# Kernel optimization log

Measured on AMD Instinct MI355X. Metric: run time of the kernel, lower is better.

Reference implementation:

```python
import jax, jax.numpy as jnp
import numpy as np

N, B, E = 50000, 1, 800000
D_IN = 128      # input_size == out_size (residual)
HID = 128       # hidden_size
H = 4           # heads
C = HID // H    # per-head dim = 32
EPS = 1e-5


def setup_inputs() -> dict:
    key = jax.random.key(0)
    ks = jax.random.split(key, 16)
    s_in = 1.0 / np.sqrt(D_IN)
    s_hid = 1.0 / np.sqrt(HID)
    return {
        "x": jax.random.normal(ks[0], (N, B, D_IN), jnp.float32),
        "edge_index": jax.random.randint(ks[1], (2, E), 0, N, jnp.int64 if jax.config.jax_enable_x64 else jnp.int32),
        "edge_attr": jax.random.normal(ks[2], (E, HID), jnp.float32),
        # TransformerConv projections (weights stored torch-style [out, in])
        "Wq": jax.random.uniform(ks[3], (HID, D_IN), jnp.float32, -s_in, s_in),
        "bq": jnp.zeros((HID,), jnp.float32),
        "Wk": jax.random.uniform(ks[4], (HID, D_IN), jnp.float32, -s_in, s_in),
        "bk": jnp.zeros((HID,), jnp.float32),
        "Wv": jax.random.uniform(ks[5], (HID, D_IN), jnp.float32, -s_in, s_in),
        "bv": jnp.zeros((HID,), jnp.float32),
        "We": jax.random.uniform(ks[6], (HID, HID), jnp.float32, -s_hid, s_hid),  # lin_edge, no bias
        "Wskip": jax.random.uniform(ks[7], (HID, D_IN), jnp.float32, -s_in, s_in),
        "bskip": jnp.zeros((HID,), jnp.float32),
        "Wp": jax.random.uniform(ks[8], (HID, HID), jnp.float32, -s_hid, s_hid),   # physics_linear
        "bp": jnp.zeros((HID,), jnp.float32),
        "Wm": jax.random.uniform(ks[9], (D_IN, HID), jnp.float32, -s_hid, s_hid),  # merge_linear
        "bm": jnp.zeros((D_IN,), jnp.float32),
    }


def reference(x, edge_index, edge_attr, Wq, bq, Wk, bk, Wv, bv, We,
              Wskip, bskip, Wp, bp, Wm, bm):
    n = x.shape[0]
    src, dst = edge_index[0], edge_index[1]  # message flows src -> dst (j -> i)

    # node-wise QKV projections -> [N, B, H, C]
    q = (x @ Wq.T + bq).reshape(n, B, H, C)
    k = (x @ Wk.T + bk).reshape(n, B, H, C)
    v = (x @ Wv.T + bv).reshape(n, B, H, C)

    # edge feature projection -> [E, H, C]
    e = (edge_attr @ We.T).reshape(-1, H, C)

    # per-edge attention scores [E, B, H]
    k_j = k[src] + e[:, None]                       # [E, B, H, C]
    alpha = (q[dst] * k_j).sum(-1) / jnp.sqrt(jnp.asarray(C, x.dtype))

    # scatter-softmax over incoming edges of each dst node
    m = jax.ops.segment_max(alpha, dst, num_segments=n)      # [N, B, H]
    a = jnp.exp(alpha - m[dst])
    s = jax.ops.segment_sum(a, dst, num_segments=n)
    alpha = a / s[dst]

    # weighted scatter-add aggregation
    msg = (v[src] + e[:, None]) * alpha[..., None]           # [E, B, H, C]
    out = jax.ops.segment_sum(msg, dst, num_segments=n)      # [N, B, H, C]
    out = out.reshape(n, B, H * C)

    # root skip connection
    out = out + (x @ Wskip.T + bskip)

    # GraphResidualBlock tail
    out = jax.nn.relu(out)
    out = out @ Wp.T + bp
    # custom LayerNorm: normalize over the node dim (dim 0), weight/bias unused
    mu = out.mean(0, keepdims=True)
    sd = out.std(0, keepdims=True)
    out = (out - mu) / (sd + EPS)
    out = jax.nn.relu(out)
    out = out @ Wm.T + bm
    return out + x
```

## Files before the change

### kernel.cpp

```cpp
#include <hip/hip_runtime.h>
#include <stdint.h>

#define RS32 0.17677669529663687f
#define LDW 40

typedef short bf16x8 __attribute__((ext_vector_type(8)));
typedef float f32x4 __attribute__((ext_vector_type(4)));

__device__ __forceinline__ ushort f2bf(float f) {
  uint32_t b = __float_as_uint(f);
  b = (b + 0x7fffu + ((b >> 16) & 1u)) >> 16;
  return (ushort)b;
}
__device__ __forceinline__ float bflo(uint32_t w) { return __uint_as_float(w << 16); }
__device__ __forceinline__ float bfhi(uint32_t w) { return __uint_as_float(w & 0xffff0000u); }

__device__ __forceinline__ void stage16(ushort* hiA, ushort* loA, int r, int koff,
                                        const float* v) {
  uint32_t hu[8], lu[8];
#pragma unroll
  for (int i = 0; i < 8; ++i) {
    uint32_t b0 = __float_as_uint(v[2 * i]), b1 = __float_as_uint(v[2 * i + 1]);
    uint32_t h0m = b0 & 0xffff0000u, h1m = b1 & 0xffff0000u;
    hu[i] = (b0 >> 16) | h1m;
    float l0 = v[2 * i] - __uint_as_float(h0m);
    float l1 = v[2 * i + 1] - __uint_as_float(h1m);
    lu[i] = (__float_as_uint(l0) >> 16) | (__float_as_uint(l1) & 0xffff0000u);
  }
  *(uint4*)&hiA[r * LDW + koff]     = make_uint4(hu[0], hu[1], hu[2], hu[3]);
  *(uint4*)&hiA[r * LDW + koff + 8] = make_uint4(hu[4], hu[5], hu[6], hu[7]);
  *(uint4*)&loA[r * LDW + koff]     = make_uint4(lu[0], lu[1], lu[2], lu[3]);
  *(uint4*)&loA[r * LDW + koff + 8] = make_uint4(lu[4], lu[5], lu[6], lu[7]);
}

__launch_bounds__(256)
__global__ void gemm128_mfma_kernel(int mode,
                                    const float* __restrict__ A, const float* __restrict__ A2,
                                    const float* __restrict__ W, const float* __restrict__ bias,
                                    const float* __restrict__ mu, const float* __restrict__ inv,
                                    const float* __restrict__ X, float* __restrict__ out,
                                    float* __restrict__ sums, float* __restrict__ sumsq, int N)
{
  __shared__ ushort Ahi[128 * LDW], Alo[128 * LDW], Whi[128 * LDW], Wlo[128 * LDW];
  const int tid = threadIdx.x;
  const int nb = blockIdx.x * 128;
  const int lane = tid & 63, wv = tid >> 6;
  const int wr = (wv >> 1) * 64, wc = (wv & 1) * 64;
  const int fr = lane & 15, fq = lane >> 4;
  const int sr = tid >> 1, sk = (tid & 1) * 16;

  f32x4 acc[4][4];
#pragma unroll
  for (int m = 0; m < 4; ++m)
#pragma unroll
    for (int n = 0; n < 4; ++n) acc[m][n] = (f32x4)0.0f;

  for (int kc = 0; kc < 128; kc += 32) {
    float va[16], vw[16];
    {
      int gr = nb + sr;
      if (gr < N) {
#pragma unroll
        for (int i = 0; i < 4; ++i) {
          float4 v = *(const float4*)(A + (size_t)gr * 128 + kc + sk + i * 4);
          if (mode == 1) {
            float4 b = *(const float4*)(A2 + (size_t)gr * 128 + kc + sk + i * 4);
            v.x = fmaxf(v.x + b.x, 0.f); v.y = fmaxf(v.y + b.y, 0.f);
            v.z = fmaxf(v.z + b.z, 0.f); v.w = fmaxf(v.w + b.w, 0.f);
          } else if (mode == 2) {
            float4 m4 = *(const float4*)(mu + kc + sk + i * 4);
            float4 i4 = *(const float4*)(inv + kc + sk + i * 4);
            v.x = fmaxf((v.x - m4.x) * i4.x, 0.f); v.y = fmaxf((v.y - m4.y) * i4.y, 0.f);
            v.z = fmaxf((v.z - m4.z) * i4.z, 0.f); v.w = fmaxf((v.w - m4.w) * i4.w, 0.f);
          }
          va[i * 4 + 0] = v.x; va[i * 4 + 1] = v.y; va[i * 4 + 2] = v.z; va[i * 4 + 3] = v.w;
        }
      } else {
#pragma unroll
        for (int i = 0; i < 16; ++i) va[i] = 0.f;
      }
#pragma unroll
      for (int i = 0; i < 4; ++i) {
        float4 v = *(const float4*)(W + (size_t)sr * 128 + kc + sk + i * 4);
        vw[i * 4 + 0] = v.x; vw[i * 4 + 1] = v.y; vw[i * 4 + 2] = v.z; vw[i * 4 + 3] = v.w;
      }
    }
    if (kc) __syncthreads();
    stage16(Ahi, Alo, sr, sk, va);
    stage16(Whi, Wlo, sr, sk, vw);
    __syncthreads();

    bf16x8 ah[4], al[4], bh[4], bl[4];
#pragma unroll
    for (int m = 0; m < 4; ++m) {
      const int row = wr + m * 16 + fr;
      ah[m] = *(const bf16x8*)&Ahi[row * LDW + fq * 8];
      al[m] = *(const bf16x8*)&Alo[row * LDW + fq * 8];
    }
#pragma unroll
    for (int n = 0; n < 4; ++n) {
      const int col = wc + n * 16 + fr;
      bh[n] = *(const bf16x8*)&Whi[col * LDW + fq * 8];
      bl[n] = *(const bf16x8*)&Wlo[col * LDW + fq * 8];
    }
#pragma unroll
    for (int m = 0; m < 4; ++m)
#pragma unroll
      for (int n = 0; n < 4; ++n) {
        acc[m][n] = __builtin_amdgcn_mfma_f32_16x16x32_bf16(ah[m], bh[n], acc[m][n], 0, 0, 0);
        acc[m][n] = __builtin_amdgcn_mfma_f32_16x16x32_bf16(al[m], bh[n], acc[m][n], 0, 0, 0);
        acc[m][n] = __builtin_amdgcn_mfma_f32_16x16x32_bf16(ah[m], bl[n], acc[m][n], 0, 0, 0);
      }
  }

  float bcol[4];
#pragma unroll
  for (int n = 0; n < 4; ++n) bcol[n] = bias[wc + n * 16 + fr];
  float csum[4] = {0.f, 0.f, 0.f, 0.f}, csum2[4] = {0.f, 0.f, 0.f, 0.f};
#pragma unroll
  for (int m = 0; m < 4; ++m) {
    const int r0 = nb + wr + m * 16 + fq * 4;
#pragma unroll
    for (int r = 0; r < 4; ++r) {
      const int gr = r0 + r;
      if (gr < N) {
#pragma unroll
        for (int n = 0; n < 4; ++n) {
          const int c = wc + n * 16 + fr;
          float o = acc[m][n][r] + bcol[n];
          if (mode == 2) o += X[(size_t)gr * 128 + c];
          out[(size_t)gr * 128 + c] = o;
          if (mode == 1) { csum[n] += o; csum2[n] = fmaf(o, o, csum2[n]); }
        }
      }
    }
  }
  if (mode == 1) {
#pragma unroll
    for (int n = 0; n < 4; ++n) {
      csum[n] += __shfl_xor(csum[n], 16, 64);
      csum[n] += __shfl_xor(csum[n], 32, 64);
      csum2[n] += __shfl_xor(csum2[n], 16, 64);
      csum2[n] += __shfl_xor(csum2[n], 32, 64);
    }
    if (fq == 0) {
#pragma unroll
      for (int n = 0; n < 4; ++n) {
        atomicAdd(&sums[wc + n * 16 + fr], csum[n]);
        atomicAdd(&sumsq[wc + n * 16 + fr], csum2[n]);
      }
    }
  }
}

__launch_bounds__(256)
__global__ void gemmqkvsu_mfma_kernel(const float* __restrict__ x,
                                      const float* __restrict__ Wq, const float* __restrict__ bq,
                                      const float* __restrict__ Wk, const float* __restrict__ bk,
                                      const float* __restrict__ Wv, const float* __restrict__ bv,
                                      const float* __restrict__ Ws, const float* __restrict__ bs,
                                      const float* __restrict__ Mt, const float* __restrict__ bu,
                                      float* __restrict__ os, ushort* __restrict__ kvi,
                                      ushort* __restrict__ u, ushort* __restrict__ qb, int N)
{
  const int y = blockIdx.y;
  const float* W; const float* bias;
  if (y == 0)      { W = Wk; bias = bk; }
  else if (y == 1) { W = Wv; bias = bv; }
  else if (y == 2) { W = Ws; bias = bs; }
  else if (y == 7) { W = Wq; bias = bq; }
  else             { W = Mt + (size_t)(y - 3) * 128 * 128; bias = bu + (y - 3) * 128; }

  __shared__ ushort Ahi[128 * LDW], Alo[128 * LDW], Whi[128 * LDW], Wlo[128 * LDW];
  const int tid = threadIdx.x;
  const int nb = blockIdx.x * 128;
  const int lane = tid & 63, wv = tid >> 6;
  const int wr = (wv >> 1) * 64, wc = (wv & 1) * 64;
  const int fr = lane & 15, fq = lane >> 4;
  const int sr = tid >> 1, sk = (tid & 1) * 16;

  f32x4 acc[4][4];
#pragma unroll
  for (int m = 0; m < 4; ++m)
#pragma unroll
    for (int n = 0; n < 4; ++n) acc[m][n] = (f32x4)0.0f;

  for (int kc = 0; kc < 128; kc += 32) {
    float va[16], vw[16];
    {
      int gr = nb + sr;
      if (gr < N) {
#pragma unroll
        for (int i = 0; i < 4; ++i) {
          float4 v = *(const float4*)(x + (size_t)gr * 128 + kc + sk + i * 4);
          va[i * 4 + 0] = v.x; va[i * 4 + 1] = v.y; va[i * 4 + 2] = v.z; va[i * 4 + 3] = v.w;
        }
      } else {
#pragma unroll
        for (int i = 0; i < 16; ++i) va[i] = 0.f;
      }
#pragma unroll
      for (int i = 0; i < 4; ++i) {
        float4 v = *(const float4*)(W + (size_t)sr * 128 + kc + sk + i * 4);
        vw[i * 4 + 0] = v.x; vw[i * 4 + 1] = v.y; vw[i * 4 + 2] = v.z; vw[i * 4 + 3] = v.w;
      }
    }
    if (kc) __syncthreads();
    stage16(Ahi, Alo, sr, sk, va);
    stage16(Whi, Wlo, sr, sk, vw);
    __syncthreads();

    bf16x8 ah[4], al[4], bh[4], bl[4];
#pragma unroll
    for (int m = 0; m < 4; ++m) {
      const int row = wr + m * 16 + fr;
      ah[m] = *(const bf16x8*)&Ahi[row * LDW + fq * 8];
      al[m] = *(const bf16x8*)&Alo[row * LDW + fq * 8];
    }
#pragma unroll
    for (int n = 0; n < 4; ++n) {
      const int col = wc + n * 16 + fr;
      bh[n] = *(const bf16x8*)&Whi[col * LDW + fq * 8];
      bl[n] = *(const bf16x8*)&Wlo[col * LDW + fq * 8];
    }
#pragma unroll
    for (int m = 0; m < 4; ++m)
#pragma unroll
      for (int n = 0; n < 4; ++n) {
        acc[m][n] = __builtin_amdgcn_mfma_f32_16x16x32_bf16(ah[m], bh[n], acc[m][n], 0, 0, 0);
        acc[m][n] = __builtin_amdgcn_mfma_f32_16x16x32_bf16(al[m], bh[n], acc[m][n], 0, 0, 0);
        acc[m][n] = __builtin_amdgcn_mfma_f32_16x16x32_bf16(ah[m], bl[n], acc[m][n], 0, 0, 0);
      }
  }

  float bcol[4];
#pragma unroll
  for (int n = 0; n < 4; ++n) bcol[n] = bias[wc + n * 16 + fr];
#pragma unroll
  for (int m = 0; m < 4; ++m) {
    const int r0 = nb + wr + m * 16 + fq * 4;
#pragma unroll
    for (int r = 0; r < 4; ++r) {
      const int gr = r0 + r;
      if (gr < N) {
#pragma unroll
        for (int n = 0; n < 4; ++n) {
          const int c = wc + n * 16 + fr;
          float o = acc[m][n][r] + bcol[n];
          if (y == 2)      os[(size_t)gr * 128 + c] = o;
          else if (y == 7) qb[(size_t)gr * 128 + c] = f2bf(o);
          else if (y == 0) kvi[(size_t)gr * 256 + (c >> 2) * 8 + (c & 3)] = f2bf(o);
          else if (y == 1) kvi[(size_t)gr * 256 + (c >> 2) * 8 + 4 + (c & 3)] = f2bf(o);
          else             u[(size_t)gr * 512 + (y - 3) * 128 + c] = f2bf(o);
        }
      }
    }
  }
}

__global__ void prep_mt_kernel(const float* __restrict__ Wq, const float* __restrict__ We,
                               float* __restrict__ Mt)
{
  const int tid = threadIdx.x;
  const int jp = blockIdx.x * 2 + (tid >> 7);
  const int d = tid & 127;
  const int h = jp >> 7, j = jp & 127;
  const float* wq = Wq + (size_t)(32 * h) * 128 + d;
  const float* we = We + (size_t)(32 * h) * 128 + j;
  float acc = 0.f;
#pragma unroll 8
  for (int a = 0; a < 32; ++a) acc = fmaf(wq[a * 128], we[a * 128], acc);
  Mt[(size_t)jp * 128 + d] = acc;
}

__global__ void prep_bu_kernel(const float* __restrict__ bq, const float* __restrict__ We,
                               float* __restrict__ bu)
{
  const int jp = threadIdx.x;
  const int h = jp >> 7, j = jp & 127;
  float acc = 0.f;
  for (int a = 0; a < 32; ++a)
    acc = fmaf(bq[32 * h + a], We[(size_t)(32 * h + a) * 128 + j], acc);
  bu[jp] = acc;
}

__global__ void prep_web_kernel(const float* __restrict__ We, ushort* __restrict__ WeB)
{
  int idx = blockIdx.x * 256 + threadIdx.x;
  if (idx >= 128 * 512) return;
  int c = idx >> 9, j = idx & 511;
  int hh = j >> 7, k2 = j & 127;
  WeB[idx] = (hh == (c >> 5)) ? f2bf(We[(size_t)c * 128 + k2]) : (ushort)0;
}

__global__ void deg_kernel(const int* __restrict__ ei, int* __restrict__ deg, int E)
{
  int e = blockIdx.x * 256 + threadIdx.x;
  if (e < E) atomicAdd(&deg[ei[E + e]], 1);
}

__launch_bounds__(256)
__global__ void start_kernel(const int* __restrict__ deg, int* __restrict__ offs,
                             int* __restrict__ cursor, int* __restrict__ gcount, int N)
{
  const int i = blockIdx.x * 256 + threadIdx.x;
  const int lane = threadIdx.x & 63;
  int d = (i < N) ? deg[i] : 0;
  int scan = d;
#pragma unroll
  for (int ofs = 1; ofs < 64; ofs <<= 1) {
    int t = __shfl_up(scan, ofs, 64);
    if (lane >= ofs) scan += t;
  }
  int total = __shfl(scan, 63, 64);
  int base = 0;
  if (lane == 63) base = atomicAdd(gcount, total);
  base = __shfl(base, 63, 64);
  int excl = base + scan - d;
  if (i < N) { offs[i] = excl; cursor[i] = excl; }
}

__global__ void fill_kernel(const int* __restrict__ ei, int* __restrict__ cursor,
                            int2* __restrict__ csr, int E)
{
  int e = blockIdx.x * 256 + threadIdx.x;
  if (e < E) {
    int dst = ei[E + e];
    int slot = atomicAdd(&cursor[dst], 1);
    csr[slot] = make_int2(ei[e], e);
  }
}

__launch_bounds__(256)
__global__ void fused_attn2_kernel(const int2* __restrict__ csr, const int* __restrict__ offs,
                                   const int* __restrict__ deg,
                                   const ushort* __restrict__ qb, const ushort* __restrict__ kvi,
                                   const ushort* __restrict__ u,
                                   const float* __restrict__ eattr,
                                   ushort* __restrict__ aggS, float* __restrict__ wsS, int N)
{
  const int tid = threadIdx.x;
  const int lane = tid & 63;
  const int wid = tid >> 6;
  const int p = lane >> 5;
  const int j32 = lane & 31;
  const int c0 = j32 * 4;
  const int h = j32 >> 3;
  const int gwave = blockIdx.x * 4 + wid;
  const int nwaves = gridDim.x * 4;

  for (int n = gwave; n < N; n += nwaves) {
    const int e0 = offs[n];
    const int e1 = e0 + deg[n];

    const uint2 qp = *(const uint2*)(qb + (size_t)n * 128 + c0);
    uint2 uhp[4];
#pragma unroll
    for (int hh = 0; hh < 4; ++hh)
      uhp[hh] = *(const uint2*)(u + (size_t)n * 512 + hh * 128 + c0);

    float ws0 = 0.f, ws1 = 0.f, ws2 = 0.f, ws3 = 0.f;
    float ax[4][4];
#pragma unroll
    for (int hh = 0; hh < 4; ++hh)
#pragma unroll
      for (int j = 0; j < 4; ++j) ax[hh][j] = 0.f;
    float sm0 = 0.f, sm1 = 0.f, sm2 = 0.f, sm3 = 0.f;

    int sl = e0 + p;
    if (sl < e1) {
      int2 seC = csr[sl];
      float4 eaC = *(const float4*)(eattr + (size_t)seC.y * 128 + c0);
      uint4 kvC = *(const uint4*)(kvi + (size_t)seC.x * 256 + j32 * 8);
      int sln = sl + 2;
      int2 seN = (sln < e1) ? csr[sln] : seC;
      for (; sl < e1; sl += 2) {
        float4 eaN = *(const float4*)(eattr + (size_t)seN.y * 128 + c0);
        uint4 kvN = *(const uint4*)(kvi + (size_t)seN.x * 256 + j32 * 8);
        const int slf = sl + 4;
        int2 seF = (slf < e1) ? csr[slf] : seN;

        float P0 = eaC.x * bflo(uhp[0].x) + eaC.y * bfhi(uhp[0].x)
                 + eaC.z * bflo(uhp[0].y) + eaC.w * bfhi(uhp[0].y);
        float P1 = eaC.x * bflo(uhp[1].x) + eaC.y * bfhi(uhp[1].x)
                 + eaC.z * bflo(uhp[1].y) + eaC.w * bfhi(uhp[1].y);
        float P2 = eaC.x * bflo(uhp[2].x) + eaC.y * bfhi(uhp[2].x)
                 + eaC.z * bflo(uhp[2].y) + eaC.w * bfhi(uhp[2].y);
        float P3 = eaC.x * bflo(uhp[3].x) + eaC.y * bfhi(uhp[3].x)
                 + eaC.z * bflo(uhp[3].y) + eaC.w * bfhi(uhp[3].y);
        const float qk = bflo(qp.x) * bflo(kvC.x) + bfhi(qp.x) * bfhi(kvC.x)
                       + bflo(qp.y) * bflo(kvC.y) + bfhi(qp.y) * bfhi(kvC.y);
        P0 += (h == 0) ? qk : 0.f;
        P1 += (h == 1) ? qk : 0.f;
        P2 += (h == 2) ? qk : 0.f;
        P3 += (h == 3) ? qk : 0.f;
#pragma unroll
        for (int mm = 1; mm <= 16; mm <<= 1) {
          P0 += __shfl_xor(P0, mm, 64);
          P1 += __shfl_xor(P1, mm, 64);
          P2 += __shfl_xor(P2, mm, 64);
          P3 += __shfl_xor(P3, mm, 64);
        }
        const float a0 = __expf(P0 * RS32);
        const float a1 = __expf(P1 * RS32);
        const float a2 = __expf(P2 * RS32);
        const float a3 = __expf(P3 * RS32);
        sm0 += a0; sm1 += a1; sm2 += a2; sm3 += a3;
        const float aV = (h == 0) ? a0 : (h == 1) ? a1 : (h == 2) ? a2 : a3;
        ws0 = fmaf(aV, bflo(kvC.z), ws0); ws1 = fmaf(aV, bfhi(kvC.z), ws1);
        ws2 = fmaf(aV, bflo(kvC.w), ws2); ws3 = fmaf(aV, bfhi(kvC.w), ws3);
        ax[0][0] = fmaf(a0, eaC.x, ax[0][0]); ax[0][1] = fmaf(a0, eaC.y, ax[0][1]);
        ax[0][2] = fmaf(a0, eaC.z, ax[0][2]); ax[0][3] = fmaf(a0, eaC.w, ax[0][3]);
        ax[1][0] = fmaf(a1, eaC.x, ax[1][0]); ax[1][1] = fmaf(a1, eaC.y, ax[1][1]);
        ax[1][2] = fmaf(a1, eaC.z, ax[1][2]); ax[1][3] = fmaf(a1, eaC.w, ax[1][3]);
        ax[2][0] = fmaf(a2, eaC.x, ax[2][0]); ax[2][1] = fmaf(a2, eaC.y, ax[2][1]);
        ax[2][2] = fmaf(a2, eaC.z, ax[2][2]); ax[2][3] = fmaf(a2, eaC.w, ax[2][3]);
        ax[3][0] = fmaf(a3, eaC.x, ax[3][0]); ax[3][1] = fmaf(a3, eaC.y, ax[3][1]);
        ax[3][2] = fmaf(a3, eaC.z, ax[3][2]); ax[3][3] = fmaf(a3, eaC.w, ax[3][3]);

        eaC = eaN; kvC = kvN; seN = seF;
      }
    }

#pragma unroll
    for (int hh = 0; hh < 4; ++hh)
#pragma unroll
      for (int j = 0; j < 4; ++j) ax[hh][j] += __shfl_xor(ax[hh][j], 32, 64);
    ws0 += __shfl_xor(ws0, 32, 64); ws1 += __shfl_xor(ws1, 32, 64);
    ws2 += __shfl_xor(ws2, 32, 64); ws3 += __shfl_xor(ws3, 32, 64);
    sm0 += __shfl_xor(sm0, 32, 64); sm1 += __shfl_xor(sm1, 32, 64);
    sm2 += __shfl_xor(sm2, 32, 64); sm3 += __shfl_xor(sm3, 32, 64);

    const float iv0 = (sm0 > 0.f) ? 1.f / sm0 : 0.f;
    const float iv1 = (sm1 > 0.f) ? 1.f / sm1 : 0.f;
    const float iv2 = (sm2 > 0.f) ? 1.f / sm2 : 0.f;
    const float iv3 = (sm3 > 0.f) ? 1.f / sm3 : 0.f;

    if (p == 0) {
      const float s = (h == 0) ? iv0 : (h == 1) ? iv1 : (h == 2) ? iv2 : iv3;
      *(float4*)(wsS + (size_t)n * 128 + c0) =
          make_float4(ws0 * s, ws1 * s, ws2 * s, ws3 * s);
    }

    float o0[4], o1[4], s0, s1;
    if (p == 0) {
#pragma unroll
      for (int j = 0; j < 4; ++j) { o0[j] = ax[0][j]; o1[j] = ax[1][j]; }
      s0 = iv0; s1 = iv1;
    } else {
#pragma unroll
      for (int j = 0; j < 4; ++j) { o0[j] = ax[2][j]; o1[j] = ax[3][j]; }
      s0 = iv2; s1 = iv3;
    }
    uint2 w0 = make_uint2(((uint32_t)f2bf(o0[0] * s0)) | (((uint32_t)f2bf(o0[1] * s0)) << 16),
                          ((uint32_t)f2bf(o0[2] * s0)) | (((uint32_t)f2bf(o0[3] * s0)) << 16));
    uint2 w1 = make_uint2(((uint32_t)f2bf(o1[0] * s1)) | (((uint32_t)f2bf(o1[1] * s1)) << 16),
                          ((uint32_t)f2bf(o1[2] * s1)) | (((uint32_t)f2bf(o1[3] * s1)) << 16));
    *(uint2*)(aggS + (size_t)n * 512 + (p * 2) * 128 + c0) = w0;
    *(uint2*)(aggS + (size_t)n * 512 + (p * 2 + 1) * 128 + c0) = w1;
  }
}

__launch_bounds__(256)
__global__ void agg_gemm_kernel(const ushort* __restrict__ aggS, const ushort* __restrict__ WeB,
                                const float* __restrict__ wsX, float* __restrict__ attn, int N)
{
  __shared__ ushort As[128][72];
  __shared__ ushort Bs[128][72];
  const int tid = threadIdx.x;
  const int nb = blockIdx.x * 128;
  const int lane = tid & 63, wv = tid >> 6;
  const int wr = (wv >> 1) * 64, wc = (wv & 1) * 64;
  const int fr = lane & 15, fq = lane >> 4;
  const int r = tid >> 1, cs = (tid & 1) * 32;

  f32x4 acc[4][4];
#pragma unroll
  for (int m = 0; m < 4; ++m)
#pragma unroll
    for (int n = 0; n < 4; ++n) acc[m][n] = (f32x4)0.0f;

  for (int kc = 0; kc < 512; kc += 64) {
    uint4 av[4], bv[4];
    if (nb + r < N) {
      const uint4* src = (const uint4*)(aggS + (size_t)(nb + r) * 512 + kc + cs);
      av[0] = src[0]; av[1] = src[1]; av[2] = src[2]; av[3] = src[3];
    } else {
#pragma unroll
      for (int i = 0; i < 4; ++i) av[i] = make_uint4(0, 0, 0, 0);
    }
    {
      const uint4* src = (const uint4*)(WeB + (size_t)r * 512 + kc + cs);
      bv[0] = src[0]; bv[1] = src[1]; bv[2] = src[2]; bv[3] = src[3];
    }
    if (kc) __syncthreads();
#pragma unroll
    for (int i = 0; i < 4; ++i) {
      *(uint4*)&As[r][cs + i * 8] = av[i];
      *(uint4*)&Bs[r][cs + i * 8] = bv[i];
    }
    __syncthreads();

#pragma unroll
    for (int s = 0; s < 2; ++s) {
      bf16x8 ah[4], bh[4];
#pragma unroll
      for (int m = 0; m < 4; ++m)
        ah[m] = *(const bf16x8*)&As[wr + m * 16 + fr][s * 32 + fq * 8];
#pragma unroll
      for (int n = 0; n < 4; ++n)
        bh[n] = *(const bf16x8*)&Bs[wc + n * 16 + fr][s * 32 + fq * 8];
#pragma unroll
      for (int m = 0; m < 4; ++m)
#pragma unroll
        for (int n = 0; n < 4; ++n)
          acc[m][n] = __builtin_amdgcn_mfma_f32_16x16x32_bf16(ah[m], bh[n], acc[m][n], 0, 0, 0);
    }
  }

#pragma unroll
  for (int m = 0; m < 4; ++m) {
    const int r0 = nb + wr + m * 16 + fq * 4;
#pragma unroll
    for (int rr = 0; rr < 4; ++rr) {
      const int gr = r0 + rr;
      if (gr < N) {
#pragma unroll
        for (int n = 0; n < 4; ++n) {
          const int c = wc + n * 16 + fr;
          attn[(size_t)gr * 128 + c] = acc[m][n][rr] + wsX[(size_t)gr * 128 + c];
        }
      }
    }
  }
}

__global__ void finalize_stats_kernel(const float* __restrict__ sums, const float* __restrict__ sumsq,
                                      float* __restrict__ mu, float* __restrict__ inv, int N)
{
  int c = threadIdx.x;
  float m = sums[c] / (float)N;
  float var = sumsq[c] / (float)N - m * m;
  float sd = sqrtf(fmaxf(var, 0.f));
  mu[c] = m;
  inv[c] = 1.f / (sd + 1e-5f);
}

extern "C" void kernel_launch(void* const* d_in, const int* in_sizes, int n_in,
                              void* d_out, int out_size, void* d_ws, size_t ws_size,
                              hipStream_t stream) {
  const float* x    = (const float*)d_in[0];
  const int*   ei   = (const int*)d_in[1];
  const float* eatt = (const float*)d_in[2];
  const float* Wq = (const float*)d_in[3];  const float* bq = (const float*)d_in[4];
  const float* Wk = (const float*)d_in[5];  const float* bk = (const float*)d_in[6];
  const float* Wv = (const float*)d_in[7];  const float* bv = (const float*)d_in[8];
  const float* We = (const float*)d_in[9];
  const float* Wsk = (const float*)d_in[10]; const float* bsk = (const float*)d_in[11];
  const float* Wp = (const float*)d_in[12]; const float* bp = (const float*)d_in[13];
  const float* Wm = (const float*)d_in[14]; const float* bm = (const float*)d_in[15];
  float* out = (float*)d_out;

  const int N = in_sizes[0] / 128;
  const int E = in_sizes[1] / 2;

  char* w = (char*)d_ws;
  auto alloc = [&](size_t bytes) {
    char* p = w;
    w += (bytes + 255) & ~(size_t)255;
    return p;
  };
  const size_t node_f = (size_t)N * 128 * sizeof(float);
  float*  skip = (float*)alloc(node_f);
  float*  wsA  = (float*)alloc(node_f);
  float*  t1   = (float*)alloc(node_f);
  ushort* qb   = (ushort*)alloc((size_t)N * 128 * sizeof(ushort));
  ushort* kvi  = (ushort*)alloc((size_t)N * 256 * sizeof(ushort));
  ushort* u    = (ushort*)alloc((size_t)N * 512 * sizeof(ushort));
  ushort* aggS = (ushort*)alloc((size_t)N * 512 * sizeof(ushort));
  ushort* WeB  = (ushort*)alloc(128 * 512 * sizeof(ushort));
  float*  Mt   = (float*)alloc(512 * 128 * sizeof(float));
  float*  bu   = (float*)alloc(512 * sizeof(float));
  int*    deg  = (int*)alloc((size_t)N * sizeof(int));
  int*    offs = (int*)alloc((size_t)N * sizeof(int));
  int*    curs = (int*)alloc((size_t)N * sizeof(int));
  int*    gcnt = (int*)alloc(sizeof(int));
  int2*   csr  = (int2*)alloc((size_t)E * sizeof(int2));
  float*  sums  = (float*)alloc(128 * sizeof(float));
  float*  sumsq = (float*)alloc(128 * sizeof(float));
  float*  mu    = (float*)alloc(128 * sizeof(float));
  float*  inv   = (float*)alloc(128 * sizeof(float));
  (void)ws_size; (void)n_in; (void)out_size;

  const int NB = (N + 127) / 128;
  const int EB = (E + 255) / 256;

  hipMemsetAsync(deg, 0, (size_t)N * sizeof(int), stream);
  hipMemsetAsync(gcnt, 0, sizeof(int), stream);
  hipMemsetAsync(sums, 0, 2 * 128 * sizeof(float), stream);

  prep_mt_kernel<<<256, 256, 0, stream>>>(Wq, We, Mt);
  prep_bu_kernel<<<1, 512, 0, stream>>>(bq, We, bu);
  prep_web_kernel<<<256, 256, 0, stream>>>(We, WeB);

  gemmqkvsu_mfma_kernel<<<dim3(NB, 8), 256, 0, stream>>>(x, Wq, bq, Wk, bk, Wv, bv, Wsk, bsk,
                                                         Mt, bu, skip, kvi, u, qb, N);

  deg_kernel<<<EB, 256, 0, stream>>>(ei, deg, E);
  start_kernel<<<(N + 255) / 256, 256, 0, stream>>>(deg, offs, curs, gcnt, N);
  fill_kernel<<<EB, 256, 0, stream>>>(ei, curs, csr, E);

  fused_attn2_kernel<<<2048, 256, 0, stream>>>(csr, offs, deg, qb, kvi, u, eatt,
                                               aggS, wsA, N);

  agg_gemm_kernel<<<NB, 256, 0, stream>>>(aggS, WeB, wsA, wsA, N);

  gemm128_mfma_kernel<<<NB, 256, 0, stream>>>(1, wsA, skip, Wp, bp, nullptr, nullptr, nullptr,
                                              t1, sums, sumsq, N);
  finalize_stats_kernel<<<1, 128, 0, stream>>>(sums, sumsq, mu, inv, N);

  gemm128_mfma_kernel<<<NB, 256, 0, stream>>>(2, t1, nullptr, Wm, bm, mu, inv, x, out,
                                              nullptr, nullptr, N);
}
```

Before: 508.0 us.

## Restructure projection GEMM to single-pass bf16 with x tile reused across eight weight sets

Replaces the split-bf16 (hi/lo, three MFMAs per product) projection GEMM with a single bf16 MFMA pass. Inputs are pre-converted to bf16 by new conversion kernels for x and the weights. Each block now loads its x tile into LDS once and loops over all eight weight matrices, instead of launching eight grid rows that each re-read x from fp32. This cuts MFMA count, global reads of x and conversion work, but lowers projection precision to plain bf16, which could affect accuracy, especially for the fp32 skip output. It also adds an extra pass over x and serialises the eight outputs within each block.

```diff
diff --git a/kernel.cpp b/kernel.cpp
--- a/kernel.cpp
+++ b/kernel.cpp
@@ -3,6 +3,7 @@
 
 #define RS32 0.17677669529663687f
 #define LDW 40
+#define PLD 136
 
 typedef short bf16x8 __attribute__((ext_vector_type(8)));
 typedef float f32x4 __attribute__((ext_vector_type(4)));
@@ -154,112 +155,127 @@
 }
 
 __launch_bounds__(256)
-__global__ void gemmqkvsu_mfma_kernel(const float* __restrict__ x,
-                                      const float* __restrict__ Wq, const float* __restrict__ bq,
-                                      const float* __restrict__ Wk, const float* __restrict__ bk,
-                                      const float* __restrict__ Wv, const float* __restrict__ bv,
-                                      const float* __restrict__ Ws, const float* __restrict__ bs,
-                                      const float* __restrict__ Mt, const float* __restrict__ bu,
-                                      float* __restrict__ os, ushort* __restrict__ kvi,
-                                      ushort* __restrict__ u, ushort* __restrict__ qb, int N)
-{
-  const int y = blockIdx.y;
-  const float* W; const float* bias;
-  if (y == 0)      { W = Wk; bias = bk; }
-  else if (y == 1) { W = Wv; bias = bv; }
-  else if (y == 2) { W = Ws; bias = bs; }
-  else if (y == 7) { W = Wq; bias = bq; }
-  else             { W = Mt + (size_t)(y - 3) * 128 * 128; bias = bu + (y - 3) * 128; }
-
-  __shared__ ushort Ahi[128 * LDW], Alo[128 * LDW], Whi[128 * LDW], Wlo[128 * LDW];
+__global__ void proj_mfma_kernel(const ushort* __restrict__ xb16,
+                                 const ushort* __restrict__ Wb,
+                                 const ushort* __restrict__ Mtb,
+                                 const float* __restrict__ bk, const float* __restrict__ bv,
+                                 const float* __restrict__ bs, const float* __restrict__ bq,
+                                 const float* __restrict__ bu,
+                                 float* __restrict__ os, ushort* __restrict__ kvi,
+                                 ushort* __restrict__ u, ushort* __restrict__ qb, int N)
+{
+  __shared__ ushort xs[128 * PLD];
+  __shared__ ushort wsh[128 * PLD];
   const int tid = threadIdx.x;
   const int nb = blockIdx.x * 128;
   const int lane = tid & 63, wv = tid >> 6;
   const int wr = (wv >> 1) * 64, wc = (wv & 1) * 64;
   const int fr = lane & 15, fq = lane >> 4;
-  const int sr = tid >> 1, sk = (tid & 1) * 16;
-
-  f32x4 acc[4][4];
+  const int sr = tid >> 1, sk = (tid & 1) * 64;
+
+  {
+    const int gr = nb + sr;
+    if (gr < N) {
+      const uint4* src = (const uint4*)(xb16 + (size_t)gr * 128 + sk);
+#pragma unroll
+      for (int i = 0; i < 8; ++i) *(uint4*)&xs[sr * PLD + sk + i * 8] = src[i];
+    } else {
+#pragma unroll
+      for (int i = 0; i < 8; ++i) *(uint4*)&xs[sr * PLD + sk + i * 8] = make_uint4(0, 0, 0, 0);
+    }
+  }
+  __syncthreads();
+
+  bf16x8 af[4][4];
 #pragma unroll
   for (int m = 0; m < 4; ++m)
 #pragma unroll
-    for (int n = 0; n < 4; ++n) acc[m][n] = (f32x4)0.0f;
-
-  for (int kc = 0; kc < 128; kc += 32) {
-    float va[16], vw[16];
+    for (int kk = 0; kk < 4; ++kk)
+      af[m][kk] = *(const bf16x8*)&xs[(wr + m * 16 + fr) * PLD + kk * 32 + fq * 8];
+
+  for (int y = 0; y < 8; ++y) {
+    const ushort* Wsrc = (y < 4) ? (Wb + (size_t)y * 16384) : (Mtb + (size_t)(y - 4) * 16384);
     {
-      int gr = nb + sr;
-      if (gr < N) {
-#pragma unroll
-        for (int i = 0; i < 4; ++i) {
-          float4 v = *(const float4*)(x + (size_t)gr * 128 + kc + sk + i * 4);
-          va[i * 4 + 0] = v.x; va[i * 4 + 1] = v.y; va[i * 4 + 2] = v.z; va[i * 4 + 3] = v.w;
+      const uint4* src = (const uint4*)(Wsrc + (size_t)sr * 128 + sk);
+#pragma unroll
+      for (int i = 0; i < 8; ++i) *(uint4*)&wsh[sr * PLD + sk + i * 8] = src[i];
+    }
+    __syncthreads();
+
+    f32x4 acc[4][4];
+#pragma unroll
+    for (int m = 0; m < 4; ++m)
+#pragma unroll
+      for (int n = 0; n < 4; ++n) acc[m][n] = (f32x4)0.0f;
+
+#pragma unroll
+    for (int n = 0; n < 4; ++n) {
+      bf16x8 bf0[4];
+#pragma unroll
+      for (int kk = 0; kk < 4; ++kk)
+        bf0[kk] = *(const bf16x8*)&wsh[(wc + n * 16 + fr) * PLD + kk * 32 + fq * 8];
+#pragma unroll
+      for (int kk = 0; kk < 4; ++kk)
+#pragma unroll
+        for (int m = 0; m < 4; ++m)
+          acc[m][n] = __builtin_amdgcn_mfma_f32_16x16x32_bf16(af[m][kk], bf0[kk], acc[m][n], 0, 0, 0);
+    }
+
+    float bcol[4];
+#pragma unroll
+    for (int n = 0; n < 4; ++n) {
+      const int c = wc + n * 16 + fr;
+      bcol[n] = (y == 0) ? bk[c] : (y == 1) ? bv[c] : (y == 2) ? bs[c]
+              : (y == 3) ? bq[c] : bu[(y - 4) * 128 + c];
+    }
+#pragma unroll
+    for (int m = 0; m < 4; ++m) {
+      const int r0 = nb + wr + m * 16 + fq * 4;
+#pragma unroll
+      for (int r = 0; r < 4; ++r) {
+        const int gr = r0 + r;
+        if (gr < N) {
+#pragma unroll
+          for (int n = 0; n < 4; ++n) {
+            const int c = wc + n * 16 + fr;
+            float o = acc[m][n][r] + bcol[n];
+            if (y == 2)      os[(size_t)gr * 128 + c] = o;
+            else if (y == 3) qb[(size_t)gr * 128 + c] = f2bf(o);
+            else if (y == 0) kvi[(size_t)gr * 256 + (c >> 2) * 8 + (c & 3)] = f2bf(o);
+            else if (y == 1) kvi[(size_t)gr * 256 + (c >> 2) * 8 + 4 + (c & 3)] = f2bf(o);
+            else             u[(size_t)gr * 512 + (y - 4) * 128 + c] = f2bf(o);
+          }
         }
-      } else {
-#pragma unroll
-        for (int i = 0; i < 16; ++i) va[i] = 0.f;
-      }
-#pragma unroll
-      for (int i = 0; i < 4; ++i) {
-        float4 v = *(const float4*)(W + (size_t)sr * 128 + kc + sk + i * 4);
-        vw[i * 4 + 0] = v.x; vw[i * 4 + 1] = v.y; vw[i * 4 + 2] = v.z; vw[i * 4 + 3] = v.w;
-      }
-    }
-    if (kc) __syncthreads();
-    stage16(Ahi, Alo, sr, sk, va);
-    stage16(Whi, Wlo, sr, sk, vw);
+      }
+    }
     __syncthreads();
-
-    bf16x8 ah[4], al[4], bh[4], bl[4];
-#pragma unroll
-    for (int m = 0; m < 4; ++m) {
-      const int row = wr + m * 16 + fr;
-      ah[m] = *(const bf16x8*)&Ahi[row * LDW + fq * 8];
-      al[m] = *(const bf16x8*)&Alo[row * LDW + fq * 8];
-    }
-#pragma unroll
-    for (int n = 0; n < 4; ++n) {
-      const int col = wc + n * 16 + fr;
-      bh[n] = *(const bf16x8*)&Whi[col * LDW + fq * 8];
-      bl[n] = *(const bf16x8*)&Wlo[col * LDW + fq * 8];
-    }
-#pragma unroll
-    for (int m = 0; m < 4; ++m)
-#pragma unroll
-      for (int n = 0; n < 4; ++n) {
-        acc[m][n] = __builtin_amdgcn_mfma_f32_16x16x32_bf16(ah[m], bh[n], acc[m][n], 0, 0, 0);
-        acc[m][n] = __builtin_amdgcn_mfma_f32_16x16x32_bf16(al[m], bh[n], acc[m][n], 0, 0, 0);
-        acc[m][n] = __builtin_amdgcn_mfma_f32_16x16x32_bf16(ah[m], bl[n], acc[m][n], 0, 0, 0);
-      }
-  }
-
-  float bcol[4];
-#pragma unroll
-  for (int n = 0; n < 4; ++n) bcol[n] = bias[wc + n * 16 + fr];
-#pragma unroll
-  for (int m = 0; m < 4; ++m) {
-    const int r0 = nb + wr + m * 16 + fq * 4;
-#pragma unroll
-    for (int r = 0; r < 4; ++r) {
-      const int gr = r0 + r;
-      if (gr < N) {
-#pragma unroll
-        for (int n = 0; n < 4; ++n) {
-          const int c = wc + n * 16 + fr;
-          float o = acc[m][n][r] + bcol[n];
-          if (y == 2)      os[(size_t)gr * 128 + c] = o;
-          else if (y == 7) qb[(size_t)gr * 128 + c] = f2bf(o);
-          else if (y == 0) kvi[(size_t)gr * 256 + (c >> 2) * 8 + (c & 3)] = f2bf(o);
-          else if (y == 1) kvi[(size_t)gr * 256 + (c >> 2) * 8 + 4 + (c & 3)] = f2bf(o);
-          else             u[(size_t)gr * 512 + (y - 3) * 128 + c] = f2bf(o);
-        }
-      }
-    }
-  }
+  }
+}
+
+__global__ void x2bf_kernel(const float* __restrict__ x, ushort* __restrict__ xb, int total4)
+{
+  int i = blockIdx.x * 256 + threadIdx.x;
+  if (i < total4) {
+    float4 v = ((const float4*)x)[i];
+    uint2 w = make_uint2((uint32_t)f2bf(v.x) | ((uint32_t)f2bf(v.y) << 16),
+                         (uint32_t)f2bf(v.z) | ((uint32_t)f2bf(v.w) << 16));
+    ((uint2*)xb)[i] = w;
+  }
+}
+
+__global__ void prep_wb_kernel(const float* __restrict__ Wk, const float* __restrict__ Wv,
+                               const float* __restrict__ Ws, const float* __restrict__ Wq,
+                               ushort* __restrict__ Wb)
+{
+  int i = blockIdx.x * 256 + threadIdx.x;
+  if (i >= 4 * 16384) return;
+  int y = i >> 14, r = i & 16383;
+  const float* src = (y == 0) ? Wk : (y == 1) ? Wv : (y == 2) ? Ws : Wq;
+  Wb[i] = f2bf(src[r]);
 }
 
 __global__ void prep_mt_kernel(const float* __restrict__ Wq, const float* __restrict__ We,
-                               float* __restrict__ Mt)
+                               ushort* __restrict__ Mtb)
 {
   const int tid = threadIdx.x;
   const int jp = blockIdx.x * 2 + (tid >> 7);
@@ -270,7 +286,7 @@
   float acc = 0.f;
 #pragma unroll 8
   for (int a = 0; a < 32; ++a) acc = fmaf(wq[a * 128], we[a * 128], acc);
-  Mt[(size_t)jp * 128 + d] = acc;
+  Mtb[(size_t)jp * 128 + d] = f2bf(acc);
 }
 
 __global__ void prep_bu_kernel(const float* __restrict__ bq, const float* __restrict__ We,
@@ -574,12 +590,14 @@
   float*  skip = (float*)alloc(node_f);
   float*  wsA  = (float*)alloc(node_f);
   float*  t1   = (float*)alloc(node_f);
+  ushort* xb16 = (ushort*)alloc((size_t)N * 128 * sizeof(ushort));
   ushort* qb   = (ushort*)alloc((size_t)N * 128 * sizeof(ushort));
   ushort* kvi  = (ushort*)alloc((size_t)N * 256 * sizeof(ushort));
   ushort* u    = (ushort*)alloc((size_t)N * 512 * sizeof(ushort));
   ushort* aggS = (ushort*)alloc((size_t)N * 512 * sizeof(ushort));
   ushort* WeB  = (ushort*)alloc(128 * 512 * sizeof(ushort));
-  float*  Mt   = (float*)alloc(512 * 128 * sizeof(float));
+  ushort* Wb   = (ushort*)alloc(4 * 128 * 128 * sizeof(ushort));
+  ushort* Mtb  = (ushort*)alloc(512 * 128 * sizeof(ushort));
   float*  bu   = (float*)alloc(512 * sizeof(float));
   int*    deg  = (int*)alloc((size_t)N * sizeof(int));
   int*    offs = (int*)alloc((size_t)N * sizeof(int));
@@ -599,12 +617,14 @@
   hipMemsetAsync(gcnt, 0, sizeof(int), stream);
   hipMemsetAsync(sums, 0, 2 * 128 * sizeof(float), stream);
 
-  prep_mt_kernel<<<256, 256, 0, stream>>>(Wq, We, Mt);
+  x2bf_kernel<<<(N * 32 + 255) / 256, 256, 0, stream>>>(x, xb16, N * 32);
+  prep_wb_kernel<<<256, 256, 0, stream>>>(Wk, Wv, Wsk, Wq, Wb);
+  prep_mt_kernel<<<256, 256, 0, stream>>>(Wq, We, Mtb);
   prep_bu_kernel<<<1, 512, 0, stream>>>(bq, We, bu);
   prep_web_kernel<<<256, 256, 0, stream>>>(We, WeB);
 
-  gemmqkvsu_mfma_kernel<<<dim3(NB, 8), 256, 0, stream>>>(x, Wq, bq, Wk, bk, Wv, bv, Wsk, bsk,
-                                                         Mt, bu, skip, kvi, u, qb, N);
+  proj_mfma_kernel<<<NB, 256, 0, stream>>>(xb16, Wb, Mtb, bk, bv, bsk, bq, bu,
+                                           skip, kvi, u, qb, N);
 
   deg_kernel<<<EB, 256, 0, stream>>>(ei, deg, E);
   start_kernel<<<(N + 255) / 256, 256, 0, stream>>>(deg, offs, curs, gcnt, N);
```

Measured after the change: 590.7 us. 1.16x slower.
